# Performance work log

Measured on AMD Instinct MI355X. Metric: run time of the kernel, lower is better.

Reference implementation:

```python
import jax, jax.numpy as jnp
import numpy as np

B, N, DX, DZ, L = 512, 32, 78, 64, 1000

def _gcn_norm(A):
    # PyG gcn_norm: add remaining self loops (fill 1), symmetric D^-1/2 (A+I) D^-1/2
    n = A.shape[-1]
    A_hat = jnp.maximum(A, jnp.eye(n, dtype=A.dtype))
    dinv = jax.lax.rsqrt(A_hat.sum(-1))
    return A_hat * dinv[..., :, None] * dinv[..., None, :]

def _bn(h, g, b, eps=1e-5):
    # BatchNorm1d, training-mode batch statistics (torch default module state)
    m = jnp.mean(h, 0)
    v = jnp.var(h, 0)
    return (h - m) * jax.lax.rsqrt(v + eps) * g + b

def _conv(h, W, b):  # h [B,C,L], W [O,I,K], valid padding + ReLU (Conv1dReLU)
    y = jax.lax.conv_general_dilated(h, W, (1,), 'VALID', dimension_numbers=('NCH', 'OIH', 'NCH'))
    return jax.nn.relu(y + b[None, :, None])

def _attn(v):  # Attention.project is only Tanh in the source
    return jax.nn.softmax(jnp.tanh(v), axis=1) * v

def _forward(x, adj, target, z, dec_W0, dec_b0, dec_g0, dec_be0, dec_W1, dec_b1, dec_g1, dec_be1,
             gW1, gb1, gW2, gb2, gW3, gb3, fcg1_W, fcg1_b, fcg2_W, fcg2_b, emb,
             c10_W, c10_b, c20_W, c20_b, c21_W, c21_b, c30_W, c30_b, c31_W, c31_b, c32_W, c32_b,
             prot_W, prot_b, fc1_W, fc1_b, fc2_W, fc2_b, out_W, out_b):
    Bn = B * N
    # frozen conditional VAE decoder -> augmented features (detached)
    zc = jnp.concatenate([z.reshape(Bn, DZ), x.reshape(Bn, DX)], axis=-1)
    h = jax.nn.relu(_bn(zc @ dec_W0 + dec_b0, dec_g0, dec_be0))
    aug = jnp.tanh(_bn(h @ dec_W1 + dec_b1, dec_g1, dec_be1))
    aug = jax.lax.stop_gradient(aug).reshape(B, N, DX)
    X = jnp.concatenate([aug, x], axis=-1)  # [B,N,156]
    # 1-hop / 2-hop / 3-hop adjacency patterns (spspmm -> binary power patterns)
    A1 = _gcn_norm(adj)
    A2p = (adj @ adj > 0).astype(adj.dtype)
    A3p = (A2p @ adj > 0).astype(adj.dtype)
    A2 = _gcn_norm(A2p)
    A3 = _gcn_norm(A3p)
    gcn = lambda A, hh, W, b: jax.nn.relu(A @ (hh @ W) + b)
    h1 = gcn(A1, X, gW1, gb1)
    h2 = gcn(A1, h1, gW2, gb2)
    h3 = gcn(A1, h2, gW3, gb3)
    h5 = gcn(A2, gcn(A2, X, gW1, gb1), gW2, gb2)
    h6 = gcn(A3, X, gW1, gb1)
    hg = jnp.max(jnp.concatenate([h3, h5, h6], axis=-1), axis=1)  # gmp -> [B,1092]
    xg = jax.nn.relu(hg @ fcg1_W + fcg1_b) @ fcg2_W + fcg2_b  # dropout = identity (eval)
    xg = _attn(xg)
    # protein branch
    e = jnp.transpose(emb[target], (0, 2, 1))  # [B,128,1000]
    f1 = jnp.max(_conv(e, c10_W, c10_b), axis=-1)
    f2 = jnp.max(_conv(_conv(e, c20_W, c20_b), c21_W, c21_b), axis=-1)
    f3 = jnp.max(_conv(_conv(_conv(e, c30_W, c30_b), c31_W, c31_b), c32_W, c32_b), axis=-1)
    xt = _attn(jnp.concatenate([f1, f2, f3], axis=-1) @ prot_W + prot_b)
    xc = jnp.concatenate([xg, xt], axis=-1)
    xc = jax.nn.relu(xc @ fc1_W + fc1_b)
    xc = jax.nn.relu(xc @ fc2_W + fc2_b)
    return xc @ out_W + out_b

def setup_inputs():
    key = jax.random.key(0)
    ks = iter(jax.random.split(key, 64))
    def w(shape, s=0.05):
        return jax.random.normal(next(ks), shape, dtype=jnp.float32) * s
    x = jax.random.normal(next(ks), (B, N, DX), dtype=jnp.float32)
    r = jax.random.uniform(next(ks), (B, N, N))
    up = jnp.triu((r < 0.08).astype(jnp.float32), 1)
    adj = up + jnp.swapaxes(up, 1, 2)  # symmetric, no self loops, avg degree ~5
    target = jax.random.randint(next(ks), (B, L), 0, 26, dtype=jnp.int32)
    z = jax.random.normal(next(ks), (B, N, DZ), dtype=jnp.float32)
    emb = w((26, 128), 1.0).at[0].set(0.0)  # padding_idx=0
    return dict(x=x, adj=adj, target=target, z=z,
        dec_W0=w((DZ + DX, 256)), dec_b0=jnp.zeros(256), dec_g0=jnp.ones(256), dec_be0=jnp.zeros(256),
        dec_W1=w((256, DX)), dec_b1=jnp.zeros(DX), dec_g1=jnp.ones(DX), dec_be1=jnp.zeros(DX),
        gW1=w((156, 156)), gb1=jnp.zeros(156), gW2=w((156, 312)), gb2=jnp.zeros(312),
        gW3=w((312, 624)), gb3=jnp.zeros(624),
        fcg1_W=w((1092, 1024)), fcg1_b=jnp.zeros(1024), fcg2_W=w((1024, 128)), fcg2_b=jnp.zeros(128),
        emb=emb,
        c10_W=w((96, 128, 3)), c10_b=jnp.zeros(96),
        c20_W=w((96, 128, 3)), c20_b=jnp.zeros(96), c21_W=w((96, 96, 3)), c21_b=jnp.zeros(96),
        c30_W=w((96, 128, 3)), c30_b=jnp.zeros(96), c31_W=w((96, 96, 3)), c31_b=jnp.zeros(96),
        c32_W=w((96, 96, 3)), c32_b=jnp.zeros(96),
        prot_W=w((288, 128)), prot_b=jnp.zeros(128),
        fc1_W=w((256, 1024)), fc1_b=jnp.zeros(1024), fc2_W=w((1024, 512)), fc2_b=jnp.zeros(512),
        out_W=w((512, 1)), out_b=jnp.zeros(1))

def reference(x, adj, target, z, dec_W0, dec_b0, dec_g0, dec_be0, dec_W1, dec_b1, dec_g1, dec_be1,
              gW1, gb1, gW2, gb2, gW3, gb3, fcg1_W, fcg1_b, fcg2_W, fcg2_b, emb,
              c10_W, c10_b, c20_W, c20_b, c21_W, c21_b, c30_W, c30_b, c31_W, c31_b, c32_W, c32_b,
              prot_W, prot_b, fc1_W, fc1_b, fc2_W, fc2_b, out_W, out_b):
    return _forward(x, adj, target, z, dec_W0, dec_b0, dec_g0, dec_be0, dec_W1, dec_b1, dec_g1, dec_be1,
                    gW1, gb1, gW2, gb2, gW3, gb3, fcg1_W, fcg1_b, fcg2_W, fcg2_b, emb,
                    c10_W, c10_b, c20_W, c20_b, c21_W, c21_b, c30_W, c30_b, c31_W, c31_b, c32_W, c32_b,
                    prot_W, prot_b, fc1_W, fc1_b, fc2_W, fc2_b, out_W, out_b)
```

## Files before the change

### kernel.cpp

```cpp
#include <hip/hip_runtime.h>

static constexpr size_t O_H0    = 0;
static constexpr size_t O_H1P   = 4194304;
static constexpr size_t O_X     = 5473216;
static constexpr size_t O_A1    = 8029120;
static constexpr size_t O_A2    = 8553408;
static constexpr size_t O_A3    = 9077696;
static constexpr size_t O_H4    = 9601984;
static constexpr size_t O_H6    = 12157888;
static constexpr size_t O_H1W2  = 14713792;
static constexpr size_t O_H2    = 19825600;
static constexpr size_t O_H2W3  = 24937408;
static constexpr size_t O_H3    = 35161024;
static constexpr size_t O_HG    = 45384640;
static constexpr size_t O_FCG1O = 45943744;
static constexpr size_t O_M     = 46468032;
static constexpr size_t O_F     = 46535424;
static constexpr size_t O_V     = 46682880;
static constexpr size_t O_XC    = 46748416;
static constexpr size_t O_FC1O  = 46879488;
static constexpr size_t O_FC2O  = 47403776;
static constexpr size_t O_PART  = 47665920;
static constexpr size_t O_MV    = 47698688;
static constexpr size_t O_BT21  = 47699712;
static constexpr size_t O_BT31  = 47727360;
static constexpr size_t O_W32T  = 47755008;
static constexpr size_t O_XW1  = O_H0;
static constexpr size_t O_SK   = O_H0;
static constexpr size_t O_H1   = O_X;
static constexpr size_t O_H4W2 = O_H1W2;
static constexpr size_t O_H5   = O_H2W3;
static constexpr size_t O_R10  = O_H1W2;
static constexpr size_t O_R20  = O_H1W2 + 1687296;
static constexpr size_t O_R30  = O_H1W2 + 3374592;
static constexpr size_t O_N21  = O_H2W3;
static constexpr size_t O_N31  = O_H2W3 + 5061888;

template<int AMODE, int ACT>
__global__ __launch_bounds__(256) void gemm_k(
    const float* __restrict__ A, const float* __restrict__ Bm,
    const float* __restrict__ bias, float* __restrict__ C,
    int M, int N, int K, const float* __restrict__ A2)
{
  __shared__ __align__(16) float sA[16 * 68];
  __shared__ __align__(16) float sB[16 * 68];
  const int tid = threadIdx.x;
  const int m0 = blockIdx.y * 64, n0 = blockIdx.x * 64;
  const int tx = tid & 15, ty = tid >> 4;
  float acc[4][4] = {};
  for (int k0 = 0; k0 < K; k0 += 16) {
#pragma unroll
    for (int s2 = 0; s2 < 4; s2++) {
      int idx = tid + s2 * 256;
      int am = idx >> 4, ak = idx & 15;
      int gm = m0 + am, gk = k0 + ak;
      float va = 0.f;
      if (gm < M && gk < K) {
        if (AMODE == 0) va = A[(size_t)gm * K + gk];
        else            va = (gk < 64) ? A[gm * 64 + gk] : A2[gm * 78 + gk - 64];
      }
      sA[ak * 68 + am] = va;
      int bk2 = idx >> 6, bn = idx & 63;
      int gk2 = k0 + bk2, gn = n0 + bn;
      float vb = 0.f;
      if (gk2 < K && gn < N) vb = Bm[(size_t)gk2 * N + gn];
      sB[bk2 * 68 + bn] = vb;
    }
    __syncthreads();
#pragma unroll
    for (int kk = 0; kk < 16; kk++) {
      const float4 a4 = *(const float4*)&sA[kk * 68 + ty * 4];
      const float4 b4 = *(const float4*)&sB[kk * 68 + tx * 4];
      const float ra[4] = {a4.x, a4.y, a4.z, a4.w};
      const float rb[4] = {b4.x, b4.y, b4.z, b4.w};
#pragma unroll
      for (int i2 = 0; i2 < 4; i2++)
#pragma unroll
        for (int j2 = 0; j2 < 4; j2++)
          acc[i2][j2] = fmaf(ra[i2], rb[j2], acc[i2][j2]);
    }
    __syncthreads();
  }
#pragma unroll
  for (int i2 = 0; i2 < 4; i2++) {
    int gm = m0 + ty * 4 + i2;
    if (gm >= M) continue;
#pragma unroll
    for (int j2 = 0; j2 < 4; j2++) {
      int gn = n0 + tx * 4 + j2;
      if (gn >= N) continue;
      float v = acc[i2][j2];
      if (bias) v += bias[gn];
      if (ACT == 1) v = fmaxf(v, 0.f);
      C[(size_t)gm * N + gn] = v;
    }
  }
}

__global__ __launch_bounds__(256) void gemm_sk(
    const float* __restrict__ A, const float* __restrict__ Bm,
    float* __restrict__ PT, int M, int N, int K, int KS)
{
  __shared__ __align__(16) float sA[16 * 68];
  __shared__ __align__(16) float sB[16 * 68];
  const int tid = threadIdx.x;
  const int m0 = blockIdx.y * 64, n0 = blockIdx.x * 64;
  const int kb = blockIdx.z * KS;
  const int ke = min(K, kb + KS);
  const int tx = tid & 15, ty = tid >> 4;
  float acc[4][4] = {};
  for (int k0 = kb; k0 < ke; k0 += 16) {
#pragma unroll
    for (int s2 = 0; s2 < 4; s2++) {
      int idx = tid + s2 * 256;
      int am = idx >> 4, ak = idx & 15;
      int gm = m0 + am, gk = k0 + ak;
      float va = 0.f;
      if (gm < M && gk < ke) va = A[(size_t)gm * K + gk];
      sA[ak * 68 + am] = va;
      int bk2 = idx >> 6, bn = idx & 63;
      int gk2 = k0 + bk2, gn = n0 + bn;
      float vb = 0.f;
      if (gk2 < ke && gn < N) vb = Bm[(size_t)gk2 * N + gn];
      sB[bk2 * 68 + bn] = vb;
    }
    __syncthreads();
#pragma unroll
    for (int kk = 0; kk < 16; kk++) {
      const float4 a4 = *(const float4*)&sA[kk * 68 + ty * 4];
      const float4 b4 = *(const float4*)&sB[kk * 68 + tx * 4];
      const float ra[4] = {a4.x, a4.y, a4.z, a4.w};
      const float rb[4] = {b4.x, b4.y, b4.z, b4.w};
#pragma unroll
      for (int i2 = 0; i2 < 4; i2++)
#pragma unroll
        for (int j2 = 0; j2 < 4; j2++)
          acc[i2][j2] = fmaf(ra[i2], rb[j2], acc[i2][j2]);
    }
    __syncthreads();
  }
  float* P = PT + (size_t)blockIdx.z * M * N;
#pragma unroll
  for (int i2 = 0; i2 < 4; i2++) {
    int gm = m0 + ty * 4 + i2;
    if (gm >= M) continue;
#pragma unroll
    for (int j2 = 0; j2 < 4; j2++) {
      int gn = n0 + tx * 4 + j2;
      if (gn >= N) continue;
      P[(size_t)gm * N + gn] = acc[i2][j2];
    }
  }
}

__global__ void skred_kernel(const float* __restrict__ PT, const float* __restrict__ bias,
                             float* __restrict__ C, int MN, int nmask, int S, int act)
{
  int i = blockIdx.x * 256 + threadIdx.x;
  if (i >= MN) return;
  float s = 0.f;
  for (int z = 0; z < S; z++) s += PT[(size_t)z * MN + i];
  if (bias) s += bias[i & nmask];
  if (act) s = fmaxf(s, 0.f);
  C[i] = s;
}

template<int AMODE, int ACT>
__global__ __launch_bounds__(256) void gemm2_k(
    const float* __restrict__ A, const float* __restrict__ Bm,
    const float* __restrict__ bias, float* __restrict__ C,
    int M, int N, int K, const float* __restrict__ A2)
{
  __shared__ __align__(16) float sA[16 * 132];
  __shared__ __align__(16) float sB[16 * 68];
  const int tid = threadIdx.x;
  const int m0 = blockIdx.y * 128, n0 = blockIdx.x * 64;
  const int tx = tid & 15, ty = tid >> 4;
// ... 210 lines not shown
  __syncthreads();
  A1o[b * 1024 + t] = ah * di * sd1[j];
  float c2 = 0.f;
#pragma unroll
  for (int k = 0; k < 32; k++) c2 += sA[i][k] * sA[k][j];
  float p2 = (c2 > 0.f) ? 1.f : 0.f;
  sP[i][j] = p2;
  float ah2 = (i == j) ? 1.f : p2;
  float rs2 = ah2;
#pragma unroll
  for (int m = 16; m >= 1; m >>= 1) rs2 += __shfl_xor(rs2, m, 32);
  float di2 = 1.f / sqrtf(rs2);
  if (j == 0) sd2[i] = di2;
  __syncthreads();
  A2o[b * 1024 + t] = ah2 * di2 * sd2[j];
  float c3 = 0.f;
#pragma unroll
  for (int k = 0; k < 32; k++) c3 += sP[i][k] * sA[k][j];
  float p3 = (c3 > 0.f) ? 1.f : 0.f;
  float ah3 = (i == j) ? 1.f : p3;
  float rs3 = ah3;
#pragma unroll
  for (int m = 16; m >= 1; m >>= 1) rs3 += __shfl_xor(rs3, m, 32);
  float di3 = 1.f / sqrtf(rs3);
  if (j == 0) sd3[i] = di3;
  __syncthreads();
  A3o[b * 1024 + t] = ah3 * di3 * sd3[j];
}

__global__ __launch_bounds__(64) void agg_kernel(const float* __restrict__ A,
    const float* __restrict__ HW, const float* __restrict__ bias,
    float* __restrict__ OUT, int C)
{
  int b = blockIdx.y;
  int c = blockIdx.x * 64 + threadIdx.x;
  __shared__ float sAd[1024];
  for (int e = threadIdx.x; e < 1024; e += 64) sAd[e] = A[b * 1024 + e];
  __syncthreads();
  if (c >= C) return;
  float hw[32];
  const float* hp = HW + (size_t)b * 32 * C + c;
#pragma unroll
  for (int m = 0; m < 32; m++) hw[m] = hp[(size_t)m * C];
  float bv = bias[c];
#pragma unroll 2
  for (int n = 0; n < 32; n++) {
    float s = bv;
#pragma unroll
    for (int m = 0; m < 32; m++) s = fmaf(sAd[n * 32 + m], hw[m], s);
    OUT[(size_t)b * 32 * C + (size_t)n * C + c] = fmaxf(s, 0.f);
  }
}

__global__ __launch_bounds__(64) void agg3_kernel(const float* __restrict__ A1,
    const float* __restrict__ A2, const float* __restrict__ A3,
    const float* __restrict__ HW, const float* __restrict__ bias,
    float* __restrict__ O1, float* __restrict__ O2, float* __restrict__ O3, int C)
{
  int b = blockIdx.y;
  int c = blockIdx.x * 64 + threadIdx.x;
  const float* A = (blockIdx.z == 0) ? A1 : ((blockIdx.z == 1) ? A2 : A3);
  float* OUT = (blockIdx.z == 0) ? O1 : ((blockIdx.z == 1) ? O2 : O3);
  __shared__ float sAd[1024];
  for (int e = threadIdx.x; e < 1024; e += 64) sAd[e] = A[b * 1024 + e];
  __syncthreads();
  if (c >= C) return;
  float hw[32];
  const float* hp = HW + (size_t)b * 32 * C + c;
#pragma unroll
  for (int m = 0; m < 32; m++) hw[m] = hp[(size_t)m * C];
  float bv = bias[c];
#pragma unroll 2
  for (int n = 0; n < 32; n++) {
    float s = bv;
#pragma unroll
    for (int m = 0; m < 32; m++) s = fmaf(sAd[n * 32 + m], hw[m], s);
    OUT[(size_t)b * 32 * C + (size_t)n * C + c] = fmaxf(s, 0.f);
  }
}

__global__ void hg_kernel(const float* __restrict__ h3, const float* __restrict__ h5,
                          const float* __restrict__ h6, float* __restrict__ HG)
{
  int b = blockIdx.y;
  int c = blockIdx.x * 256 + threadIdx.x;
  if (c >= 1092) return;
  const float* p; int stride;
  if (c < 624)      { p = h3 + (size_t)b * 32 * 624 + c;          stride = 624; }
  else if (c < 936) { p = h5 + (size_t)b * 32 * 312 + (c - 624);  stride = 312; }
  else              { p = h6 + (size_t)b * 32 * 156 + (c - 936);  stride = 156; }
  float m = p[0];
#pragma unroll 4
  for (int n = 1; n < 32; n++) m = fmaxf(m, p[(size_t)n * stride]);
  HG[b * 1092 + c] = m;
}

__global__ __launch_bounds__(64) void attn_kernel(const float* __restrict__ V,
    float* __restrict__ OUT, int ostride, int ooff)
{
  int r = blockIdx.x, lane = threadIdx.x;
  float v0 = V[r * 128 + lane], v1 = V[r * 128 + 64 + lane];
  float e0 = expf(tanhf(v0)), e1 = expf(tanhf(v1));
  float s = e0 + e1;
#pragma unroll
  for (int m = 32; m >= 1; m >>= 1) s += __shfl_xor(s, m);
  float inv = 1.f / s;
  OUT[r * ostride + ooff + lane] = e0 * inv * v0;
  OUT[r * ostride + ooff + 64 + lane] = e1 * inv * v1;
}

__global__ void mtable_kernel(const float* __restrict__ emb, const float* __restrict__ W10,
    const float* __restrict__ W20, const float* __restrict__ W30, float* __restrict__ M)
{
  int idx = blockIdx.x * 256 + threadIdx.x;
  if (idx >= 3 * 3 * 26 * 96) return;
  int o = idx % 96, tok = (idx / 96) % 26, k = (idx / (96 * 26)) % 3, cv = idx / (96 * 26 * 3);
  const float* W = (cv == 0) ? W10 : ((cv == 1) ? W20 : W30);
  float s = 0.f;
#pragma unroll 4
  for (int i = 0; i < 128; i++) s = fmaf(emb[tok * 128 + i], W[(o * 128 + i) * 3 + k], s);
  M[idx] = s;
}

__global__ void rtable_kernel(const float* __restrict__ M,
    const float* __restrict__ b1, const float* __restrict__ b2, const float* __restrict__ b3,
    float* __restrict__ R1, float* __restrict__ R2, float* __restrict__ R3)
{
  int cv = blockIdx.y;
  int idx = blockIdx.x * 256 + threadIdx.x;
  if (idx >= 17576 * 96) return;
  int o = idx % 96, g = idx / 96;
  int t0 = g / 676, t1 = (g / 26) % 26, t2 = g % 26;
  const float* Mc = M + cv * 3 * 26 * 96;
  float v = ((cv == 0) ? b1 : ((cv == 1) ? b2 : b3))[o];
  v += Mc[(0 * 26 + t0) * 96 + o] + Mc[(1 * 26 + t1) * 96 + o] + Mc[(2 * 26 + t2) * 96 + o];
  float* R = (cv == 0) ? R1 : ((cv == 1) ? R2 : R3);
  R[idx] = fmaxf(v, 0.f);
}

__global__ void wtrans3_kernel(const float* __restrict__ W21, const float* __restrict__ W31,
                               const float* __restrict__ W32,
                               float* __restrict__ O21, float* __restrict__ O31,
                               float* __restrict__ O32)
{
  int e = blockIdx.x * 256 + threadIdx.x;
  if (e >= 96 * 96 * 3) return;
  int job = blockIdx.y;
  const float* W = (job == 0) ? W21 : ((job == 1) ? W31 : W32);
  float* out = (job == 0) ? O21 : ((job == 1) ? O31 : O32);
  int o, i, k;
  if (job < 2) { i = e / 288; int r = e % 288; k = r / 96; o = r % 96; }
  else         { k = e / (96 * 96); i = (e / 96) % 96; o = e % 96; }
  out[e] = W[(o * 96 + i) * 3 + k];
}

__global__ __launch_bounds__(384) void conv3_fused(const int* __restrict__ target,
    const float* __restrict__ R10,
    const float* __restrict__ N21, const float* __restrict__ b21,
    const float* __restrict__ N31, const float* __restrict__ b31,
    const float* __restrict__ W32t, const float* __restrict__ b32, float* __restrict__ F)
{
  int b = blockIdx.y, tile = blockIdx.x;
  int l0 = tile * 64;
  int tid = threadIdx.x;
  __shared__ float sIn[96 * 67];
  __shared__ int sG[68];
  __shared__ unsigned sR[192];
  int ncols = min(66, 996 - l0);
  int n1    = min(66, 998 - l0);
  int nouts = min(64, 994 - l0);
  int ng    = min(68, 998 - l0);
  if (tid < 192) sR[tid] = 0u;
  for (int p = tid; p < ng; p += 384) {
    int t0 = target[b * 1000 + l0 + p];
    int t1 = target[b * 1000 + l0 + p + 1];
    int t2 = target[b * 1000 + l0 + p + 2];
    sG[p] = (t0 * 26 + t1) * 26 + t2;
  }
  __syncthreads();
  {
    int ig = tid % 24;
    int coff = tid / 24;
    int i4 = ig * 4;
    float4 v1m = make_float4(0.f, 0.f, 0.f, 0.f);
    float4 v2m = make_float4(0.f, 0.f, 0.f, 0.f);
    const float4 bb31 = *(const float4*)&b31[i4];
    const float4 bb21 = *(const float4*)&b21[i4];
    for (int c = coff; c < n1; c += 16) {
      float4 r1 = *(const float4*)&R10[(size_t)sG[c] * 96 + i4];
      v1m.x = fmaxf(v1m.x, r1.x); v1m.y = fmaxf(v1m.y, r1.y);
      v1m.z = fmaxf(v1m.z, r1.z); v1m.w = fmaxf(v1m.w, r1.w);
      if (c < ncols) {
        size_t r0 = (size_t)sG[c] * 3 + 0;
        size_t r1i = (size_t)sG[c + 1] * 3 + 1;
        size_t r2 = (size_t)sG[c + 2] * 3 + 2;
        float4 a0 = *(const float4*)&N31[r0 * 96 + i4];
        float4 a1 = *(const float4*)&N31[r1i * 96 + i4];
        float4 a2 = *(const float4*)&N31[r2 * 96 + i4];
        sIn[(i4 + 0) * 67 + c] = fmaxf(bb31.x + a0.x + a1.x + a2.x, 0.f);
        sIn[(i4 + 1) * 67 + c] = fmaxf(bb31.y + a0.y + a1.y + a2.y, 0.f);
        sIn[(i4 + 2) * 67 + c] = fmaxf(bb31.z + a0.z + a1.z + a2.z, 0.f);
        sIn[(i4 + 3) * 67 + c] = fmaxf(bb31.w + a0.w + a1.w + a2.w, 0.f);
        float4 c0 = *(const float4*)&N21[r0 * 96 + i4];
        float4 c1 = *(const float4*)&N21[r1i * 96 + i4];
        float4 c2 = *(const float4*)&N21[r2 * 96 + i4];
        v2m.x = fmaxf(v2m.x, bb21.x + c0.x + c1.x + c2.x);
        v2m.y = fmaxf(v2m.y, bb21.y + c0.y + c1.y + c2.y);
        v2m.z = fmaxf(v2m.z, bb21.z + c0.z + c1.z + c2.z);
        v2m.w = fmaxf(v2m.w, bb21.w + c0.w + c1.w + c2.w);
      }
    }
    atomicMax(&sR[i4 + 0], __float_as_uint(v1m.x));
    atomicMax(&sR[i4 + 1], __float_as_uint(v1m.y));
    atomicMax(&sR[i4 + 2], __float_as_uint(v1m.z));
    atomicMax(&sR[i4 + 3], __float_as_uint(v1m.w));
    atomicMax(&sR[96 + i4 + 0], __float_as_uint(fmaxf(v2m.x, 0.f)));
    atomicMax(&sR[96 + i4 + 1], __float_as_uint(fmaxf(v2m.y, 0.f)));
    atomicMax(&sR[96 + i4 + 2], __float_as_uint(fmaxf(v2m.z, 0.f)));
    atomicMax(&sR[96 + i4 + 3], __float_as_uint(fmaxf(v2m.w, 0.f)));
  }
  __syncthreads();
  if (tid < 192) {
    int which = tid / 96, i = tid % 96;
    atomicMax((unsigned int*)&F[b * 288 + which * 96 + i], sR[tid]);
  }
  int wv = __builtin_amdgcn_readfirstlane(tid >> 6);
  int lane = tid & 63;
  int obase = wv * 16;
  float acc[16];
#pragma unroll
  for (int jj = 0; jj < 16; jj++) acc[jj] = b32[obase + jj];
#pragma unroll 1
  for (int k = 0; k < 3; k++) {
#pragma unroll 4
    for (int i = 0; i < 96; i++) {
      float xv = sIn[i * 67 + lane + k];
      const float* wp = W32t + ((size_t)(k * 96 + i)) * 96 + obase;
#pragma unroll
      for (int jj = 0; jj < 16; jj++) acc[jj] = fmaf(xv, wp[jj], acc[jj]);
    }
  }
  bool lok = lane < nouts;
#pragma unroll
  for (int jj = 0; jj < 16; jj++) {
    float v = lok ? fmaxf(acc[jj], 0.f) : 0.f;
#pragma unroll
    for (int m = 32; m >= 1; m >>= 1) v = fmaxf(v, __shfl_xor(v, m));
    if (lane == 0) atomicMax((unsigned int*)&F[b * 288 + 192 + obase + jj], __float_as_uint(v));
  }
}

__global__ __launch_bounds__(256) void outdot_kernel(const float* __restrict__ X,
    const float* __restrict__ W, const float* __restrict__ bptr, float* __restrict__ out)
{
  int r = blockIdx.x * 4 + (threadIdx.x >> 6);
  int lane = threadIdx.x & 63;
  float s = 0.f;
  for (int j = lane; j < 512; j += 64) s = fmaf(X[(size_t)r * 512 + j], W[j], s);
#pragma unroll
  for (int m = 32; m >= 1; m >>= 1) s += __shfl_xor(s, m);
  if (lane == 0) out[r] = s + bptr[0];
}

static inline void gemm(hipStream_t st, int AMODE, int ACT,
                        const float* A, const float* B, const float* bias, float* C,
                        int M, int N, int K, const float* A2 = nullptr)
{
  dim3 g((N + 63) / 64, (M + 63) / 64), blk(256);
  if (AMODE == 0 && ACT == 0)      gemm_k<0, 0><<<g, blk, 0, st>>>(A, B, bias, C, M, N, K, A2);
  else if (AMODE == 0 && ACT == 1) gemm_k<0, 1><<<g, blk, 0, st>>>(A, B, bias, C, M, N, K, A2);
  else                             gemm_k<1, 0><<<g, blk, 0, st>>>(A, B, bias, C, M, N, K, A2);
}

static inline void gemm2(hipStream_t st, int AMODE, int ACT,
                         const float* A, const float* B, const float* bias, float* C,
                         int M, int N, int K, const float* A2 = nullptr)
{
  dim3 g((N + 63) / 64, (M + 127) / 128), blk(256);
  if (AMODE == 0 && ACT == 0)      gemm2_k<0, 0><<<g, blk, 0, st>>>(A, B, bias, C, M, N, K, A2);
  else if (AMODE == 0 && ACT == 1) gemm2_k<0, 1><<<g, blk, 0, st>>>(A, B, bias, C, M, N, K, A2);
  else                             gemm2_k<1, 0><<<g, blk, 0, st>>>(A, B, bias, C, M, N, K, A2);
}

static inline void gemm3(hipStream_t st, int AMODE, int ACT,
                         const float* A, const float* B, const float* bias, float* C,
                         int M, int N, int K, const float* A2 = nullptr)
{
  dim3 g((N + 127) / 128, (M + 127) / 128), blk(256);
  if (AMODE == 0 && ACT == 0)      gemm3_k<0, 0><<<g, blk, 0, st>>>(A, B, bias, C, M, N, K, A2);
  else if (AMODE == 0 && ACT == 1) gemm3_k<0, 1><<<g, blk, 0, st>>>(A, B, bias, C, M, N, K, A2);
  else                             gemm3_k<1, 0><<<g, blk, 0, st>>>(A, B, bias, C, M, N, K, A2);
}

static inline void gemm_splitk(hipStream_t st, const float* A, const float* B,
                               const float* bias, float* C, int M, int N, int K,
                               int S, int act, float* PT)
{
  int KS = (K + S - 1) / S;
  dim3 g((N + 63) / 64, (M + 63) / 64, S);
  gemm_sk<<<g, 256, 0, st>>>(A, B, PT, M, N, K, KS);
  int MN = M * N;
  skred_kernel<<<(MN + 255) / 256, 256, 0, st>>>(PT, bias, C, MN, N - 1, S, act);
}

extern "C" void kernel_launch(void* const* d_in, const int* in_sizes, int n_in,
                              void* d_out, int out_size, void* d_ws, size_t ws_size,
                              hipStream_t stream)
{
  (void)in_sizes; (void)n_in; (void)out_size; (void)ws_size;
  const float* x      = (const float*)d_in[0];
  const float* adj    = (const float*)d_in[1];
  const int*   target = (const int*)  d_in[2];
  const float* z      = (const float*)d_in[3];
  const float* dec_W0 = (const float*)d_in[4];
  const float* dec_b0 = (const float*)d_in[5];
  const float* dec_g0 = (const float*)d_in[6];
  const float* dec_be0= (const float*)d_in[7];
  const float* dec_W1 = (const float*)d_in[8];
  const float* dec_b1 = (const float*)d_in[9];
  const float* dec_g1 = (const float*)d_in[10];
  const float* dec_be1= (const float*)d_in[11];
  const float* gW1    = (const float*)d_in[12];
  const float* gb1    = (const float*)d_in[13];
  const float* gW2    = (const float*)d_in[14];
  const float* gb2    = (const float*)d_in[15];
  const float* gW3    = (const float*)d_in[16];
  const float* gb3    = (const float*)d_in[17];
  const float* fcg1_W = (const float*)d_in[18];
  const float* fcg1_b = (const float*)d_in[19];
  const float* fcg2_W = (const float*)d_in[20];
  const float* fcg2_b = (const float*)d_in[21];
  const float* emb    = (const float*)d_in[22];
  const float* c10_W  = (const float*)d_in[23];
  const float* c10_b  = (const float*)d_in[24];
  const float* c20_W  = (const float*)d_in[25];
  const float* c20_b  = (const float*)d_in[26];
  const float* c21_W  = (const float*)d_in[27];
  const float* c21_b  = (const float*)d_in[28];
  const float* c30_W  = (const float*)d_in[29];
  const float* c30_b  = (const float*)d_in[30];
  const float* c31_W  = (const float*)d_in[31];
  const float* c31_b  = (const float*)d_in[32];
  const float* c32_W  = (const float*)d_in[33];
  const float* c32_b  = (const float*)d_in[34];
  const float* prot_W = (const float*)d_in[35];
  const float* prot_b = (const float*)d_in[36];
  const float* fc1_W  = (const float*)d_in[37];
  const float* fc1_b  = (const float*)d_in[38];
  const float* fc2_W  = (const float*)d_in[39];
  const float* fc2_b  = (const float*)d_in[40];
  const float* out_W  = (const float*)d_in[41];
  const float* out_b  = (const float*)d_in[42];
  float* out = (float*)d_out;
  float* ws = (float*)d_ws;

  float* H0   = ws + O_H0;   float* H1P  = ws + O_H1P;  float* X    = ws + O_X;
  float* A1   = ws + O_A1;   float* A2   = ws + O_A2;   float* A3   = ws + O_A3;
  float* XW1  = ws + O_XW1;  float* H1   = ws + O_H1;   float* H4   = ws + O_H4;
  float* H6   = ws + O_H6;   float* H1W2 = ws + O_H1W2; float* H2   = ws + O_H2;
  float* H2W3 = ws + O_H2W3; float* H3   = ws + O_H3;   float* H4W2 = ws + O_H4W2;
  float* H5   = ws + O_H5;   float* HG   = ws + O_HG;   float* FCG1O= ws + O_FCG1O;
  float* Mt   = ws + O_M;    float* F    = ws + O_F;    float* V    = ws + O_V;
  float* XC   = ws + O_XC;   float* FC1O = ws + O_FC1O; float* FC2O = ws + O_FC2O;
  float* PS   = ws + O_PART; float* PQ   = ws + O_PART + 16384;
  float* MV   = ws + O_MV;   float* SK   = ws + O_SK;
  float* R10  = ws + O_R10;  float* R20  = ws + O_R20;  float* R30  = ws + O_R30;
  float* N21  = ws + O_N21;  float* N31  = ws + O_N31;
  float* BT21 = ws + O_BT21; float* BT31 = ws + O_BT31; float* W32T = ws + O_W32T;

  gemm2(stream, 1, 0, z, dec_W0, dec_b0, H0, 16384, 256, 142, x);
  bn_partial<<<dim3(4, 64), 256, 0, stream>>>(H0, PS, PQ, 256);
  bn_final<<<1, 256, 0, stream>>>(PS, PQ, MV, 256);
  bn_norm<<<16384, 256, 0, stream>>>(H0, H0, MV, dec_g0, dec_be0, 256, 256, 16384 * 256, 1, nullptr);
  gemm2(stream, 0, 0, H0, dec_W1, dec_b1, H1P, 16384, 78, 256);
  bn_partial<<<dim3(2, 64), 256, 0, stream>>>(H1P, PS, PQ, 78);
  bn_final<<<1, 256, 0, stream>>>(PS, PQ, MV, 78);
  bn_norm<<<4995, 256, 0, stream>>>(H1P, X, MV, dec_g1, dec_be1, 78, 156, 16384 * 78, 2, x);

  adj_kernel<<<512, 1024, 0, stream>>>(adj, A1, A2, A3);

  gemm3(stream, 0, 0, X, gW1, nullptr, XW1, 16384, 156, 156);
  agg3_kernel<<<dim3(3, 512, 3), 64, 0, stream>>>(A1, A2, A3, XW1, gb1, H1, H4, H6, 156);
  gemm3(stream, 0, 0, H1, gW2, nullptr, H1W2, 16384, 312, 156);
  agg_kernel<<<dim3(5, 512), 64, 0, stream>>>(A1, H1W2, gb2, H2, 312);
  gemm3(stream, 0, 0, H2, gW3, nullptr, H2W3, 16384, 624, 312);
  agg_kernel<<<dim3(10, 512), 64, 0, stream>>>(A1, H2W3, gb3, H3, 624);
  gemm3(stream, 0, 0, H4, gW2, nullptr, H4W2, 16384, 312, 156);
  agg_kernel<<<dim3(5, 512), 64, 0, stream>>>(A2, H4W2, gb2, H5, 312);
  hg_kernel<<<dim3(5, 512), 256, 0, stream>>>(H3, H5, H6, HG);

  gemm_splitk(stream, HG, fcg1_W, fcg1_b, FCG1O, 512, 1024, 1092, 4, 1, SK);
  gemm_splitk(stream, FCG1O, fcg2_W, fcg2_b, V, 512, 128, 1024, 8, 0, SK);
  attn_kernel<<<512, 64, 0, stream>>>(V, XC, 256, 0);

  hipMemsetAsync(F, 0, 512 * 288 * sizeof(float), stream);
  mtable_kernel<<<264, 256, 0, stream>>>(emb, c10_W, c20_W, c30_W, Mt);
  rtable_kernel<<<dim3(6591, 3), 256, 0, stream>>>(Mt, c10_b, c20_b, c30_b, R10, R20, R30);
  wtrans3_kernel<<<dim3(108, 3), 256, 0, stream>>>(c21_W, c31_W, c32_W, BT21, BT31, W32T);
  gemm3(stream, 0, 0, R20, BT21, nullptr, N21, 17576, 288, 96);
  gemm3(stream, 0, 0, R30, BT31, nullptr, N31, 17576, 288, 96);
  conv3_fused<<<dim3(16, 512), 384, 0, stream>>>(target, R10, N21, c21_b, N31, c31_b, W32T, c32_b, F);
  gemm_splitk(stream, F, prot_W, prot_b, V, 512, 128, 288, 4, 0, SK);
  attn_kernel<<<512, 64, 0, stream>>>(V, XC, 256, 128);

  gemm_splitk(stream, XC, fc1_W, fc1_b, FC1O, 512, 1024, 256, 2, 1, SK);
  gemm_splitk(stream, FC1O, fc2_W, fc2_b, FC2O, 512, 512, 1024, 4, 1, SK);
  outdot_kernel<<<128, 256, 0, stream>>>(FC2O, out_W, out_b, out);
}
```

Before: 1.305 ms.

## Software-pipeline conv3_fused over four tiles and vectorize split-K tile loads

```diff
diff --git a/kernel.cpp b/kernel.cpp
--- a/kernel.cpp
+++ b/kernel.cpp
@@ -36,67 +36,6 @@
 static constexpr size_t O_N21  = O_H2W3;
 static constexpr size_t O_N31  = O_H2W3 + 5061888;
 
-template<int AMODE, int ACT>
-__global__ __launch_bounds__(256) void gemm_k(
-    const float* __restrict__ A, const float* __restrict__ Bm,
-    const float* __restrict__ bias, float* __restrict__ C,
-    int M, int N, int K, const float* __restrict__ A2)
-{
-  __shared__ __align__(16) float sA[16 * 68];
-  __shared__ __align__(16) float sB[16 * 68];
-  const int tid = threadIdx.x;
-  const int m0 = blockIdx.y * 64, n0 = blockIdx.x * 64;
-  const int tx = tid & 15, ty = tid >> 4;
-  float acc[4][4] = {};
-  for (int k0 = 0; k0 < K; k0 += 16) {
-#pragma unroll
-    for (int s2 = 0; s2 < 4; s2++) {
-      int idx = tid + s2 * 256;
-      int am = idx >> 4, ak = idx & 15;
-      int gm = m0 + am, gk = k0 + ak;
-      float va = 0.f;
-      if (gm < M && gk < K) {
-        if (AMODE == 0) va = A[(size_t)gm * K + gk];
-        else            va = (gk < 64) ? A[gm * 64 + gk] : A2[gm * 78 + gk - 64];
-      }
-      sA[ak * 68 + am] = va;
-      int bk2 = idx >> 6, bn = idx & 63;
-      int gk2 = k0 + bk2, gn = n0 + bn;
-      float vb = 0.f;
-      if (gk2 < K && gn < N) vb = Bm[(size_t)gk2 * N + gn];
-      sB[bk2 * 68 + bn] = vb;
-    }
-    __syncthreads();
-#pragma unroll
-    for (int kk = 0; kk < 16; kk++) {
-      const float4 a4 = *(const float4*)&sA[kk * 68 + ty * 4];
-      const float4 b4 = *(const float4*)&sB[kk * 68 + tx * 4];
-      const float ra[4] = {a4.x, a4.y, a4.z, a4.w};
-      const float rb[4] = {b4.x, b4.y, b4.z, b4.w};
-#pragma unroll
-      for (int i2 = 0; i2 < 4; i2++)
-#pragma unroll
-        for (int j2 = 0; j2 < 4; j2++)
-          acc[i2][j2] = fmaf(ra[i2], rb[j2], acc[i2][j2]);
-    }
-    __syncthreads();
-  }
-#pragma unroll
-  for (int i2 = 0; i2 < 4; i2++) {
-    int gm = m0 + ty * 4 + i2;
-    if (gm >= M) continue;
-#pragma unroll
-    for (int j2 = 0; j2 < 4; j2++) {
-      int gn = n0 + tx * 4 + j2;
-      if (gn >= N) continue;
-      float v = acc[i2][j2];
-      if (bias) v += bias[gn];
-      if (ACT == 1) v = fmaxf(v, 0.f);
-      C[(size_t)gm * N + gn] = v;
-    }
-  }
-}
-
 __global__ __launch_bounds__(256) void gemm_sk(
     const float* __restrict__ A, const float* __restrict__ Bm,
     float* __restrict__ PT, int M, int N, int K, int KS)
@@ -108,21 +47,39 @@
   const int kb = blockIdx.z * KS;
   const int ke = min(K, kb + KS);
   const int tx = tid & 15, ty = tid >> 4;
+  const bool fullM = (m0 + 64 <= M), fullN = (n0 + 64 <= N);
   float acc[4][4] = {};
   for (int k0 = kb; k0 < ke; k0 += 16) {
-#pragma unroll
-    for (int s2 = 0; s2 < 4; s2++) {
-      int idx = tid + s2 * 256;
-      int am = idx >> 4, ak = idx & 15;
-      int gm = m0 + am, gk = k0 + ak;
-      float va = 0.f;
-      if (gm < M && gk < ke) va = A[(size_t)gm * K + gk];
-      sA[ak * 68 + am] = va;
-      int bk2 = idx >> 6, bn = idx & 63;
-      int gk2 = k0 + bk2, gn = n0 + bn;
-      float vb = 0.f;
-      if (gk2 < ke && gn < N) vb = Bm[(size_t)gk2 * N + gn];
-      sB[bk2 * 68 + bn] = vb;
+    const bool fullK = (k0 + 16 <= ke);
+    if (fullM && fullK) {
+      const int am = tid >> 2, ak = (tid & 3) * 4;
+      const float4 v = *(const float4*)&A[(size_t)(m0 + am) * K + k0 + ak];
+      sA[(ak + 0) * 68 + am] = v.x; sA[(ak + 1) * 68 + am] = v.y;
+      sA[(ak + 2) * 68 + am] = v.z; sA[(ak + 3) * 68 + am] = v.w;
+    } else {
+#pragma unroll
+      for (int s2 = 0; s2 < 4; s2++) {
+        int idx = tid + s2 * 256;
+        int am = idx >> 4, ak = idx & 15;
+        int gm = m0 + am, gk = k0 + ak;
+        float va = 0.f;
+        if (gm < M && gk < ke) va = A[(size_t)gm * K + gk];
+        sA[ak * 68 + am] = va;
+      }
+    }
+    if (fullN && fullK) {
+      const int bk = tid >> 4, bn4 = (tid & 15) * 4;
+      *(float4*)&sB[bk * 68 + bn4] = *(const float4*)&Bm[(size_t)(k0 + bk) * N + n0 + bn4];
+    } else {
+#pragma unroll
+      for (int s2 = 0; s2 < 4; s2++) {
+        int idx = tid + s2 * 256;
+        int bk2 = idx >> 6, bn = idx & 63;
+        int gk2 = k0 + bk2, gn = n0 + bn;
+        float vb = 0.f;
+        if (gk2 < ke && gn < N) vb = Bm[(size_t)gk2 * N + gn];
+        sB[bk2 * 68 + bn] = vb;
+      }
     }
     __syncthreads();
 #pragma unroll
@@ -547,93 +504,128 @@
     const float* __restrict__ N31, const float* __restrict__ b31,
     const float* __restrict__ W32t, const float* __restrict__ b32, float* __restrict__ F)
 {
-  int b = blockIdx.y, tile = blockIdx.x;
-  int l0 = tile * 64;
-  int tid = threadIdx.x;
-  __shared__ float sIn[96 * 67];
-  __shared__ int sG[68];
+  const int b = blockIdx.y;
+  const int base = blockIdx.x * 256;
+  const int tid = threadIdx.x;
+  __shared__ float sIn[2][96 * 67];
+  __shared__ int sG[260];
   __shared__ unsigned sR[192];
-  int ncols = min(66, 996 - l0);
-  int n1    = min(66, 998 - l0);
-  int nouts = min(64, 994 - l0);
-  int ng    = min(68, 998 - l0);
+  const int ngr = min(260, 998 - base);
   if (tid < 192) sR[tid] = 0u;
-  for (int p = tid; p < ng; p += 384) {
-    int t0 = target[b * 1000 + l0 + p];
-    int t1 = target[b * 1000 + l0 + p + 1];
-    int t2 = target[b * 1000 + l0 + p + 2];
+  for (int p = tid; p < ngr; p += 384) {
+    int t0 = target[b * 1000 + base + p];
+    int t1 = target[b * 1000 + base + p + 1];
+    int t2 = target[b * 1000 + base + p + 2];
     sG[p] = (t0 * 26 + t1) * 26 + t2;
   }
   __syncthreads();
-  {
-    int ig = tid % 24;
-    int coff = tid / 24;
-    int i4 = ig * 4;
-    float4 v1m = make_float4(0.f, 0.f, 0.f, 0.f);
-    float4 v2m = make_float4(0.f, 0.f, 0.f, 0.f);
-    const float4 bb31 = *(const float4*)&b31[i4];
-    const float4 bb21 = *(const float4*)&b21[i4];
-    for (int c = coff; c < n1; c += 16) {
-      float4 r1 = *(const float4*)&R10[(size_t)sG[c] * 96 + i4];
-      v1m.x = fmaxf(v1m.x, r1.x); v1m.y = fmaxf(v1m.y, r1.y);
-      v1m.z = fmaxf(v1m.z, r1.z); v1m.w = fmaxf(v1m.w, r1.w);
-      if (c < ncols) {
-        size_t r0 = (size_t)sG[c] * 3 + 0;
-        size_t r1i = (size_t)sG[c + 1] * 3 + 1;
-        size_t r2 = (size_t)sG[c + 2] * 3 + 2;
-        float4 a0 = *(const float4*)&N31[r0 * 96 + i4];
-        float4 a1 = *(const float4*)&N31[r1i * 96 + i4];
-        float4 a2 = *(const float4*)&N31[r2 * 96 + i4];
-        sIn[(i4 + 0) * 67 + c] = fmaxf(bb31.x + a0.x + a1.x + a2.x, 0.f);
-        sIn[(i4 + 1) * 67 + c] = fmaxf(bb31.y + a0.y + a1.y + a2.y, 0.f);
-        sIn[(i4 + 2) * 67 + c] = fmaxf(bb31.z + a0.z + a1.z + a2.z, 0.f);
-        sIn[(i4 + 3) * 67 + c] = fmaxf(bb31.w + a0.w + a1.w + a2.w, 0.f);
-        float4 c0 = *(const float4*)&N21[r0 * 96 + i4];
-        float4 c1 = *(const float4*)&N21[r1i * 96 + i4];
-        float4 c2 = *(const float4*)&N21[r2 * 96 + i4];
-        v2m.x = fmaxf(v2m.x, bb21.x + c0.x + c1.x + c2.x);
-        v2m.y = fmaxf(v2m.y, bb21.y + c0.y + c1.y + c2.y);
-        v2m.z = fmaxf(v2m.z, bb21.z + c0.z + c1.z + c2.z);
-        v2m.w = fmaxf(v2m.w, bb21.w + c0.w + c1.w + c2.w);
-      }
-    }
-    atomicMax(&sR[i4 + 0], __float_as_uint(v1m.x));
-    atomicMax(&sR[i4 + 1], __float_as_uint(v1m.y));
-    atomicMax(&sR[i4 + 2], __float_as_uint(v1m.z));
-    atomicMax(&sR[i4 + 3], __float_as_uint(v1m.w));
-    atomicMax(&sR[96 + i4 + 0], __float_as_uint(fmaxf(v2m.x, 0.f)));
-    atomicMax(&sR[96 + i4 + 1], __float_as_uint(fmaxf(v2m.y, 0.f)));
-    atomicMax(&sR[96 + i4 + 2], __float_as_uint(fmaxf(v2m.z, 0.f)));
-    atomicMax(&sR[96 + i4 + 3], __float_as_uint(fmaxf(v2m.w, 0.f)));
-  }
+
+  const int ig = tid % 24, coff = tid / 24, i4 = ig * 4;
+  const float4 bb31 = *(const float4*)&b31[i4];
+  const float4 bb21 = *(const float4*)&b21[i4];
+  float4 v1m = make_float4(0.f, 0.f, 0.f, 0.f);
+  float4 v2m = make_float4(0.f, 0.f, 0.f, 0.f);
+  const int wv = tid >> 6, lane = tid & 63;
+  const int obase = __builtin_amdgcn_readfirstlane(wv) * 16;
+  float acc[16];
+
+  int cl_ = 0; bool do1_ = false, do2_ = false;
+  int g0 = 0, g1 = 0, g2 = 0;
+  float4 r1a, a0a, a1a, a2a, c0a, c1a, c2a;
+
+#define ISSUE(tt, jj) { \
+    const int l0_ = base + 64 * (tt); \
+    const int n1_ = min(66, 998 - l0_); \
+    const int nc_ = min(66, 996 - l0_); \
+    cl_ = coff + 16 * (jj); \
+    do1_ = cl_ < n1_; do2_ = cl_ < nc_; \
+    if (do1_) { g0 = sG[64 * (tt) + cl_]; \
+      r1a = *(const float4*)&R10[(size_t)g0 * 96 + i4]; } \
+    if (do2_) { g1 = sG[64 * (tt) + cl_ + 1]; g2 = sG[64 * (tt) + cl_ + 2]; \
+      a0a = *(const float4*)&N31[((size_t)g0 * 3 + 0) * 96 + i4]; \
+      a1a = *(const float4*)&N31[((size_t)g1 * 3 + 1) * 96 + i4]; \
+      a2a = *(const float4*)&N31[((size_t)g2 * 3 + 2) * 96 + i4]; \
+      c0a = *(const float4*)&N21[((size_t)g0 * 3 + 0) * 96 + i4]; \
+      c1a = *(const float4*)&N21[((size_t)g1 * 3 + 1) * 96 + i4]; \
+      c2a = *(const float4*)&N21[((size_t)g2 * 3 + 2) * 96 + i4]; } \
+  }
+
+#define CONSUME(dst) { \
+    if (do1_) { \
+      v1m.x = fmaxf(v1m.x, r1a.x); v1m.y = fmaxf(v1m.y, r1a.y); \
+      v1m.z = fmaxf(v1m.z, r1a.z); v1m.w = fmaxf(v1m.w, r1a.w); } \
+    if (do2_) { \
+      (dst)[(i4 + 0) * 67 + cl_] = fmaxf(bb31.x + a0a.x + a1a.x + a2a.x, 0.f); \
+      (dst)[(i4 + 1) * 67 + cl_] = fmaxf(bb31.y + a0a.y + a1a.y + a2a.y, 0.f); \
+      (dst)[(i4 + 2) * 67 + cl_] = fmaxf(bb31.z + a0a.z + a1a.z + a2a.z, 0.f); \
+      (dst)[(i4 + 3) * 67 + cl_] = fmaxf(bb31.w + a0a.w + a1a.w + a2a.w, 0.f); \
+      v2m.x = fmaxf(v2m.x, bb21.x + c0a.x + c1a.x + c2a.x); \
+      v2m.y = fmaxf(v2m.y, bb21.y + c0a.y + c1a.y + c2a.y); \
+      v2m.z = fmaxf(v2m.z, bb21.z + c0a.z + c1a.z + c2a.z); \
+      v2m.w = fmaxf(v2m.w, bb21.w + c0a.w + c1a.w + c2a.w); } \
+  }
+
+#define FMAQ(src, q) { \
+    _Pragma("unroll 3") \
+    for (int k = 0; k < 3; k++) { \
+      _Pragma("unroll 4") \
+      for (int ii = 0; ii < 24; ii++) { \
+        const int i = (q) * 24 + ii; \
+        const float xv = (src)[i * 67 + lane + k]; \
+        const float* wp = W32t + ((size_t)(k * 96 + i)) * 96 + obase; \
+        _Pragma("unroll") \
+        for (int jj = 0; jj < 16; jj++) acc[jj] = fmaf(xv, wp[jj], acc[jj]); \
+      } \
+    } \
+  }
+
+  float* cur = sIn[0];
+  float* nxt = sIn[1];
+#pragma unroll
+  for (int j = 0; j < 5; j++) { ISSUE(0, j); CONSUME(cur); }
+  __syncthreads();
+
+#pragma unroll 1
+  for (int t = 0; t < 4; t++) {
+#pragma unroll
+    for (int jj = 0; jj < 16; jj++) acc[jj] = b32[obase + jj];
+    if (t < 3) {
+      ISSUE(t + 1, 0); FMAQ(cur, 0); CONSUME(nxt);
+      ISSUE(t + 1, 1); FMAQ(cur, 1); CONSUME(nxt);
+      ISSUE(t + 1, 2); FMAQ(cur, 2); CONSUME(nxt);
+      ISSUE(t + 1, 3); FMAQ(cur, 3); CONSUME(nxt);
+      ISSUE(t + 1, 4); CONSUME(nxt);
+    } else {
+      FMAQ(cur, 0); FMAQ(cur, 1); FMAQ(cur, 2); FMAQ(cur, 3);
+    }
+    const int noutst = min(64, 994 - (base + 64 * t));
+    const bool lok = lane < noutst;
+#pragma unroll
+    for (int jj = 0; jj < 16; jj++) {
+      float v = lok ? fmaxf(acc[jj], 0.f) : 0.f;
+#pragma unroll
+      for (int m = 32; m >= 1; m >>= 1) v = fmaxf(v, __shfl_xor(v, m));
+      if (lane == 0) atomicMax((unsigned int*)&F[b * 288 + 192 + obase + jj], __float_as_uint(v));
+    }
+    __syncthreads();
+    float* tmp = cur; cur = nxt; nxt = tmp;
+  }
+#undef ISSUE
+#undef CONSUME
+#undef FMAQ
+
+  atomicMax(&sR[i4 + 0], __float_as_uint(v1m.x));
+  atomicMax(&sR[i4 + 1], __float_as_uint(v1m.y));
+  atomicMax(&sR[i4 + 2], __float_as_uint(v1m.z));
+  atomicMax(&sR[i4 + 3], __float_as_uint(v1m.w));
+  atomicMax(&sR[96 + i4 + 0], __float_as_uint(fmaxf(v2m.x, 0.f)));
+  atomicMax(&sR[96 + i4 + 1], __float_as_uint(fmaxf(v2m.y, 0.f)));
+  atomicMax(&sR[96 + i4 + 2], __float_as_uint(fmaxf(v2m.z, 0.f)));
+  atomicMax(&sR[96 + i4 + 3], __float_as_uint(fmaxf(v2m.w, 0.f)));
   __syncthreads();
   if (tid < 192) {
     int which = tid / 96, i = tid % 96;
     atomicMax((unsigned int*)&F[b * 288 + which * 96 + i], sR[tid]);
-  }
-  int wv = __builtin_amdgcn_readfirstlane(tid >> 6);
-  int lane = tid & 63;
-  int obase = wv * 16;
-  float acc[16];
-#pragma unroll
-  for (int jj = 0; jj < 16; jj++) acc[jj] = b32[obase + jj];
-#pragma unroll 1
-  for (int k = 0; k < 3; k++) {
-#pragma unroll 4
-    for (int i = 0; i < 96; i++) {
-      float xv = sIn[i * 67 + lane + k];
-      const float* wp = W32t + ((size_t)(k * 96 + i)) * 96 + obase;
-#pragma unroll
-      for (int jj = 0; jj < 16; jj++) acc[jj] = fmaf(xv, wp[jj], acc[jj]);
-    }
-  }
-  bool lok = lane < nouts;
-#pragma unroll
-  for (int jj = 0; jj < 16; jj++) {
-    float v = lok ? fmaxf(acc[jj], 0.f) : 0.f;
-#pragma unroll
-    for (int m = 32; m >= 1; m >>= 1) v = fmaxf(v, __shfl_xor(v, m));
-    if (lane == 0) atomicMax((unsigned int*)&F[b * 288 + 192 + obase + jj], __float_as_uint(v));
   }
 }
 
@@ -647,16 +639,6 @@
 #pragma unroll
   for (int m = 32; m >= 1; m >>= 1) s += __shfl_xor(s, m);
   if (lane == 0) out[r] = s + bptr[0];
-}
-
-static inline void gemm(hipStream_t st, int AMODE, int ACT,
-                        const float* A, const float* B, const float* bias, float* C,
-                        int M, int N, int K, const float* A2 = nullptr)
-{
-  dim3 g((N + 63) / 64, (M + 63) / 64), blk(256);
-  if (AMODE == 0 && ACT == 0)      gemm_k<0, 0><<<g, blk, 0, st>>>(A, B, bias, C, M, N, K, A2);
-  else if (AMODE == 0 && ACT == 1) gemm_k<0, 1><<<g, blk, 0, st>>>(A, B, bias, C, M, N, K, A2);
-  else                             gemm_k<1, 0><<<g, blk, 0, st>>>(A, B, bias, C, M, N, K, A2);
 }
 
 static inline void gemm2(hipStream_t st, int AMODE, int ACT,
@@ -786,7 +768,7 @@
   wtrans3_kernel<<<dim3(108, 3), 256, 0, stream>>>(c21_W, c31_W, c32_W, BT21, BT31, W32T);
   gemm3(stream, 0, 0, R20, BT21, nullptr, N21, 17576, 288, 96);
   gemm3(stream, 0, 0, R30, BT31, nullptr, N31, 17576, 288, 96);
-  conv3_fused<<<dim3(16, 512), 384, 0, stream>>>(target, R10, N21, c21_b, N31, c31_b, W32T, c32_b, F);
+  conv3_fused<<<dim3(4, 512), 384, 0, stream>>>(target, R10, N21, c21_b, N31, c31_b, W32T, c32_b, F);
   gemm_splitk(stream, F, prot_W, prot_b, V, 512, 128, 288, 4, 0, SK);
   attn_kernel<<<512, 64, 0, stream>>>(V, XC, 256, 128);
 
```

Result: slower. 1.773 ms (+35.9%).

## Fuse global max pooling into final GCN aggregation and vectorize split-K tile loads

Applied to the files above, without the earlier changes.

```diff
diff --git a/kernel.cpp b/kernel.cpp
--- a/kernel.cpp
+++ b/kernel.cpp
@@ -29,73 +29,11 @@
 static constexpr size_t O_SK   = O_H0;
 static constexpr size_t O_H1   = O_X;
 static constexpr size_t O_H4W2 = O_H1W2;
-static constexpr size_t O_H5   = O_H2W3;
 static constexpr size_t O_R10  = O_H1W2;
 static constexpr size_t O_R20  = O_H1W2 + 1687296;
 static constexpr size_t O_R30  = O_H1W2 + 3374592;
 static constexpr size_t O_N21  = O_H2W3;
 static constexpr size_t O_N31  = O_H2W3 + 5061888;
-
-template<int AMODE, int ACT>
-__global__ __launch_bounds__(256) void gemm_k(
-    const float* __restrict__ A, const float* __restrict__ Bm,
-    const float* __restrict__ bias, float* __restrict__ C,
-    int M, int N, int K, const float* __restrict__ A2)
-{
-  __shared__ __align__(16) float sA[16 * 68];
-  __shared__ __align__(16) float sB[16 * 68];
-  const int tid = threadIdx.x;
-  const int m0 = blockIdx.y * 64, n0 = blockIdx.x * 64;
-  const int tx = tid & 15, ty = tid >> 4;
-  float acc[4][4] = {};
-  for (int k0 = 0; k0 < K; k0 += 16) {
-#pragma unroll
-    for (int s2 = 0; s2 < 4; s2++) {
-      int idx = tid + s2 * 256;
-      int am = idx >> 4, ak = idx & 15;
-      int gm = m0 + am, gk = k0 + ak;
-      float va = 0.f;
-      if (gm < M && gk < K) {
-        if (AMODE == 0) va = A[(size_t)gm * K + gk];
-        else            va = (gk < 64) ? A[gm * 64 + gk] : A2[gm * 78 + gk - 64];
-      }
-      sA[ak * 68 + am] = va;
-      int bk2 = idx >> 6, bn = idx & 63;
-      int gk2 = k0 + bk2, gn = n0 + bn;
-      float vb = 0.f;
-      if (gk2 < K && gn < N) vb = Bm[(size_t)gk2 * N + gn];
-      sB[bk2 * 68 + bn] = vb;
-    }
-    __syncthreads();
-#pragma unroll
-    for (int kk = 0; kk < 16; kk++) {
-      const float4 a4 = *(const float4*)&sA[kk * 68 + ty * 4];
-      const float4 b4 = *(const float4*)&sB[kk * 68 + tx * 4];
-      const float ra[4] = {a4.x, a4.y, a4.z, a4.w};
-      const float rb[4] = {b4.x, b4.y, b4.z, b4.w};
-#pragma unroll
-      for (int i2 = 0; i2 < 4; i2++)
-#pragma unroll
-        for (int j2 = 0; j2 < 4; j2++)
-          acc[i2][j2] = fmaf(ra[i2], rb[j2], acc[i2][j2]);
-    }
-    __syncthreads();
-  }
-#pragma unroll
-  for (int i2 = 0; i2 < 4; i2++) {
-    int gm = m0 + ty * 4 + i2;
-    if (gm >= M) continue;
-#pragma unroll
-    for (int j2 = 0; j2 < 4; j2++) {
-      int gn = n0 + tx * 4 + j2;
-      if (gn >= N) continue;
-      float v = acc[i2][j2];
-      if (bias) v += bias[gn];
-      if (ACT == 1) v = fmaxf(v, 0.f);
-      C[(size_t)gm * N + gn] = v;
-    }
-  }
-}
 
 __global__ __launch_bounds__(256) void gemm_sk(
     const float* __restrict__ A, const float* __restrict__ Bm,
@@ -108,21 +46,39 @@
   const int kb = blockIdx.z * KS;
   const int ke = min(K, kb + KS);
   const int tx = tid & 15, ty = tid >> 4;
+  const bool fullM = (m0 + 64 <= M), fullN = (n0 + 64 <= N);
   float acc[4][4] = {};
   for (int k0 = kb; k0 < ke; k0 += 16) {
-#pragma unroll
-    for (int s2 = 0; s2 < 4; s2++) {
-      int idx = tid + s2 * 256;
-      int am = idx >> 4, ak = idx & 15;
-      int gm = m0 + am, gk = k0 + ak;
-      float va = 0.f;
-      if (gm < M && gk < ke) va = A[(size_t)gm * K + gk];
-      sA[ak * 68 + am] = va;
-      int bk2 = idx >> 6, bn = idx & 63;
-      int gk2 = k0 + bk2, gn = n0 + bn;
-      float vb = 0.f;
-      if (gk2 < ke && gn < N) vb = Bm[(size_t)gk2 * N + gn];
-      sB[bk2 * 68 + bn] = vb;
+    const bool fullK = (k0 + 16 <= ke);
+    if (fullM && fullK) {
+      const int am = tid >> 2, ak = (tid & 3) * 4;
+      const float4 v = *(const float4*)&A[(size_t)(m0 + am) * K + k0 + ak];
+      sA[(ak + 0) * 68 + am] = v.x; sA[(ak + 1) * 68 + am] = v.y;
+      sA[(ak + 2) * 68 + am] = v.z; sA[(ak + 3) * 68 + am] = v.w;
+    } else {
+#pragma unroll
+      for (int s2 = 0; s2 < 4; s2++) {
+        int idx = tid + s2 * 256;
+        int am = idx >> 4, ak = idx & 15;
+        int gm = m0 + am, gk = k0 + ak;
+        float va = 0.f;
+        if (gm < M && gk < ke) va = A[(size_t)gm * K + gk];
+        sA[ak * 68 + am] = va;
+      }
+    }
+    if (fullN && fullK) {
+      const int bk = tid >> 4, bn4 = (tid & 15) * 4;
+      *(float4*)&sB[bk * 68 + bn4] = *(const float4*)&Bm[(size_t)(k0 + bk) * N + n0 + bn4];
+    } else {
+#pragma unroll
+      for (int s2 = 0; s2 < 4; s2++) {
+        int idx = tid + s2 * 256;
+        int bk2 = idx >> 6, bn = idx & 63;
+        int gk2 = k0 + bk2, gn = n0 + bn;
+        float vb = 0.f;
+        if (gk2 < ke && gn < N) vb = Bm[(size_t)gk2 * N + gn];
+        sB[bk2 * 68 + bn] = vb;
+      }
     }
     __syncthreads();
 #pragma unroll
@@ -439,15 +395,41 @@
   }
 }
 
+__global__ __launch_bounds__(64) void aggmax_kernel(const float* __restrict__ A,
+    const float* __restrict__ HW, const float* __restrict__ bias,
+    float* __restrict__ HG, int C, int off)
+{
+  int b = blockIdx.y;
+  int c = blockIdx.x * 64 + threadIdx.x;
+  __shared__ float sAd[1024];
+  for (int e = threadIdx.x; e < 1024; e += 64) sAd[e] = A[b * 1024 + e];
+  __syncthreads();
+  if (c >= C) return;
+  float hw[32];
+  const float* hp = HW + (size_t)b * 32 * C + c;
+#pragma unroll
+  for (int m = 0; m < 32; m++) hw[m] = hp[(size_t)m * C];
+  float bv = bias[c];
+  float mx = -3.4e38f;
+#pragma unroll 2
+  for (int n = 0; n < 32; n++) {
+    float s = bv;
+#pragma unroll
+    for (int m = 0; m < 32; m++) s = fmaf(sAd[n * 32 + m], hw[m], s);
+    mx = fmaxf(mx, s);
+  }
+  HG[b * 1092 + off + c] = fmaxf(mx, 0.f);
+}
+
 __global__ __launch_bounds__(64) void agg3_kernel(const float* __restrict__ A1,
     const float* __restrict__ A2, const float* __restrict__ A3,
     const float* __restrict__ HW, const float* __restrict__ bias,
-    float* __restrict__ O1, float* __restrict__ O2, float* __restrict__ O3, int C)
+    float* __restrict__ O1, float* __restrict__ O2, float* __restrict__ HG, int C)
 {
   int b = blockIdx.y;
   int c = blockIdx.x * 64 + threadIdx.x;
-  const float* A = (blockIdx.z == 0) ? A1 : ((blockIdx.z == 1) ? A2 : A3);
-  float* OUT = (blockIdx.z == 0) ? O1 : ((blockIdx.z == 1) ? O2 : O3);
+  const int zz = blockIdx.z;
+  const float* A = (zz == 0) ? A1 : ((zz == 1) ? A2 : A3);
   __shared__ float sAd[1024];
   for (int e = threadIdx.x; e < 1024; e += 64) sAd[e] = A[b * 1024 + e];
   __syncthreads();
@@ -457,29 +439,26 @@
 #pragma unroll
   for (int m = 0; m < 32; m++) hw[m] = hp[(size_t)m * C];
   float bv = bias[c];
+  if (zz < 2) {
+    float* OUT = (zz == 0) ? O1 : O2;
 #pragma unroll 2
-  for (int n = 0; n < 32; n++) {
-    float s = bv;
-#pragma unroll
-    for (int m = 0; m < 32; m++) s = fmaf(sAd[n * 32 + m], hw[m], s);
-    OUT[(size_t)b * 32 * C + (size_t)n * C + c] = fmaxf(s, 0.f);
-  }
-}
-
-__global__ void hg_kernel(const float* __restrict__ h3, const float* __restrict__ h5,
-                          const float* __restrict__ h6, float* __restrict__ HG)
-{
-  int b = blockIdx.y;
-  int c = blockIdx.x * 256 + threadIdx.x;
-  if (c >= 1092) return;
-  const float* p; int stride;
-  if (c < 624)      { p = h3 + (size_t)b * 32 * 624 + c;          stride = 624; }
-  else if (c < 936) { p = h5 + (size_t)b * 32 * 312 + (c - 624);  stride = 312; }
-  else              { p = h6 + (size_t)b * 32 * 156 + (c - 936);  stride = 156; }
-  float m = p[0];
-#pragma unroll 4
-  for (int n = 1; n < 32; n++) m = fmaxf(m, p[(size_t)n * stride]);
-  HG[b * 1092 + c] = m;
+    for (int n = 0; n < 32; n++) {
+      float s = bv;
+#pragma unroll
+      for (int m = 0; m < 32; m++) s = fmaf(sAd[n * 32 + m], hw[m], s);
+      OUT[(size_t)b * 32 * C + (size_t)n * C + c] = fmaxf(s, 0.f);
+    }
+  } else {
+    float mx = -3.4e38f;
+#pragma unroll 2
+    for (int n = 0; n < 32; n++) {
+      float s = bv;
+#pragma unroll
+      for (int m = 0; m < 32; m++) s = fmaf(sAd[n * 32 + m], hw[m], s);
+      mx = fmaxf(mx, s);
+    }
+    HG[b * 1092 + 936 + c] = fmaxf(mx, 0.f);
+  }
 }
 
 __global__ __launch_bounds__(64) void attn_kernel(const float* __restrict__ V,
@@ -647,16 +626,6 @@
 #pragma unroll
   for (int m = 32; m >= 1; m >>= 1) s += __shfl_xor(s, m);
   if (lane == 0) out[r] = s + bptr[0];
-}
-
-static inline void gemm(hipStream_t st, int AMODE, int ACT,
-                        const float* A, const float* B, const float* bias, float* C,
-                        int M, int N, int K, const float* A2 = nullptr)
-{
-  dim3 g((N + 63) / 64, (M + 63) / 64), blk(256);
-  if (AMODE == 0 && ACT == 0)      gemm_k<0, 0><<<g, blk, 0, st>>>(A, B, bias, C, M, N, K, A2);
-  else if (AMODE == 0 && ACT == 1) gemm_k<0, 1><<<g, blk, 0, st>>>(A, B, bias, C, M, N, K, A2);
-  else                             gemm_k<1, 0><<<g, blk, 0, st>>>(A, B, bias, C, M, N, K, A2);
 }
 
 static inline void gemm2(hipStream_t st, int AMODE, int ACT,
@@ -744,9 +713,9 @@
   float* H0   = ws + O_H0;   float* H1P  = ws + O_H1P;  float* X    = ws + O_X;
   float* A1   = ws + O_A1;   float* A2   = ws + O_A2;   float* A3   = ws + O_A3;
   float* XW1  = ws + O_XW1;  float* H1   = ws + O_H1;   float* H4   = ws + O_H4;
-  float* H6   = ws + O_H6;   float* H1W2 = ws + O_H1W2; float* H2   = ws + O_H2;
-  float* H2W3 = ws + O_H2W3; float* H3   = ws + O_H3;   float* H4W2 = ws + O_H4W2;
-  float* H5   = ws + O_H5;   float* HG   = ws + O_HG;   float* FCG1O= ws + O_FCG1O;
+  float* H1W2 = ws + O_H1W2; float* H2   = ws + O_H2;
+  float* H2W3 = ws + O_H2W3; float* H4W2 = ws + O_H4W2;
+  float* HG   = ws + O_HG;   float* FCG1O= ws + O_FCG1O;
   float* Mt   = ws + O_M;    float* F    = ws + O_F;    float* V    = ws + O_V;
   float* XC   = ws + O_XC;   float* FC1O = ws + O_FC1O; float* FC2O = ws + O_FC2O;
   float* PS   = ws + O_PART; float* PQ   = ws + O_PART + 16384;
@@ -767,14 +736,13 @@
   adj_kernel<<<512, 1024, 0, stream>>>(adj, A1, A2, A3);
 
   gemm3(stream, 0, 0, X, gW1, nullptr, XW1, 16384, 156, 156);
-  agg3_kernel<<<dim3(3, 512, 3), 64, 0, stream>>>(A1, A2, A3, XW1, gb1, H1, H4, H6, 156);
+  agg3_kernel<<<dim3(3, 512, 3), 64, 0, stream>>>(A1, A2, A3, XW1, gb1, H1, H4, HG, 156);
   gemm3(stream, 0, 0, H1, gW2, nullptr, H1W2, 16384, 312, 156);
   agg_kernel<<<dim3(5, 512), 64, 0, stream>>>(A1, H1W2, gb2, H2, 312);
   gemm3(stream, 0, 0, H2, gW3, nullptr, H2W3, 16384, 624, 312);
-  agg_kernel<<<dim3(10, 512), 64, 0, stream>>>(A1, H2W3, gb3, H3, 624);
+  aggmax_kernel<<<dim3(10, 512), 64, 0, stream>>>(A1, H2W3, gb3, HG, 624, 0);
   gemm3(stream, 0, 0, H4, gW2, nullptr, H4W2, 16384, 312, 156);
-  agg_kernel<<<dim3(5, 512), 64, 0, stream>>>(A2, H4W2, gb2, H5, 312);
-  hg_kernel<<<dim3(5, 512), 256, 0, stream>>>(H3, H5, H6, HG);
+  aggmax_kernel<<<dim3(5, 512), 64, 0, stream>>>(A2, H4W2, gb2, HG, 312, 624);
 
   gemm_splitk(stream, HG, fcg1_W, fcg1_b, FCG1O, 512, 1024, 1092, 4, 1, SK);
   gemm_splitk(stream, FCG1O, fcg2_W, fcg2_b, V, 512, 128, 1024, 8, 0, SK);
```

New measurement: 1.197 ms. 8.3% less time.
